# Performance work log

Measured on AMD Instinct MI355X. Metric: run time of the kernel, lower is better.

## Reference

```python
import jax, jax.numpy as jnp
import numpy as np

DIN, DK, DV, DR, NH, DMODEL = 512, 64, 64, 16, 8, 512
N = 4096
TOT = DK + DK + DV + DR  # per-head projection width = 208


def setup_inputs() -> dict:
    key = jax.random.key(0)
    k1, k2, k3, k4 = jax.random.split(key, 4)
    H = jax.random.normal(k1, (N, DIN), dtype=jnp.float32)
    D = jax.random.normal(k2, (N, N, DR), dtype=jnp.float32)
    attention_mask = jnp.zeros((N, N), dtype=jnp.float32)  # 0 = allowed
    # learned params (Linear, no bias): stored as [in, out] for x @ W
    W = jax.random.normal(k3, (DIN, NH * TOT), dtype=jnp.float32) / np.sqrt(DIN)
    Wout = jax.random.normal(k4, (NH * DV, DMODEL), dtype=jnp.float32) / np.sqrt(NH * DV)
    return {"H": H, "D": D, "attention_mask": attention_mask, "W": W, "Wout": Wout}


def reference(H, D, attention_mask, W, Wout):
    n = H.shape[0]
    # project and split into per-head Q, K, V, R: [h, n, *]
    H2 = (H @ W).reshape(n, NH, TOT).transpose(1, 0, 2)
    Q, K, V, R = jnp.split(H2, [DK, 2 * DK, 2 * DK + DV], axis=-1)
    # relative/route bias: RD[h,i,j] = sum_r R[h,i,r] * D[i,j,r]
    RD = jnp.einsum('hir,ijr->hij', R, D)
    scale = 1.0 / np.sqrt(DK + DR)
    scores = scale * (jnp.einsum('hid,hjd->hij', Q, K) + RD) + attention_mask
    probs = jax.nn.softmax(scores, axis=-1)
    ctx = jnp.einsum('hij,hjd->hid', probs, V)          # [h, n, dv]
    ctx = ctx.transpose(1, 0, 2).reshape(n, NH * DV)    # [n, h*dv]
    return ctx @ Wout                                    # [n, dmodel]
```

## Files before the change

kernel.cpp:

```cpp
#include <hip/hip_runtime.h>
#include <hip/hip_bf16.h>

#define NN 4096
#define NH 8
#define TOT 208
#define NPROJ 1664

typedef __attribute__((ext_vector_type(8))) short short8;
typedef __attribute__((ext_vector_type(4))) short short4_t;
typedef __attribute__((ext_vector_type(4))) float float4_t;

#define MFMA __builtin_amdgcn_mfma_f32_16x16x32_bf16

__device__ __forceinline__ short f2bf(float f){
  union { float f; unsigned u; } v; v.f = f;
  unsigned r = v.u + 0x7fffu + ((v.u >> 16) & 1u);
  return (short)(r >> 16);
}

__device__ __forceinline__ float bitsf(unsigned u){
  union { unsigned u; float f; } v; v.u = u; return v.f;
}

__device__ __forceinline__ short8 cvt8(float4_t a, float4_t b){
  union { short8 s; unsigned u[4]; } r;
  asm("v_cvt_pk_bf16_f32 %0, %1, %2" : "=v"(r.u[0]) : "v"(a[0]), "v"(a[1]));
  asm("v_cvt_pk_bf16_f32 %0, %1, %2" : "=v"(r.u[1]) : "v"(a[2]), "v"(a[3]));
  asm("v_cvt_pk_bf16_f32 %0, %1, %2" : "=v"(r.u[2]) : "v"(b[0]), "v"(b[1]));
  asm("v_cvt_pk_bf16_f32 %0, %1, %2" : "=v"(r.u[3]) : "v"(b[2]), "v"(b[3]));
  return r.s;
}

#define BAR() do{ \
    asm volatile("s_waitcnt lgkmcnt(0)" ::: "memory"); \
    __builtin_amdgcn_s_barrier(); \
    asm volatile("" ::: "memory"); \
  }while(0)

__global__ void k_cvt(const float* __restrict__ in, short* __restrict__ out, int n4){
  int i = blockIdx.x*256 + threadIdx.x;
  if(i >= n4) return;
  float4_t v = *(const float4_t*)(in + (size_t)i*4);
  short4_t o;
  o[0]=f2bf(v[0]); o[1]=f2bf(v[1]); o[2]=f2bf(v[2]); o[3]=f2bf(v[3]);
  *(short4_t*)(out + (size_t)i*4) = o;
}

__global__ void k_trans(const float* __restrict__ in, short* __restrict__ out, int R, int C){
  __shared__ float tile[32][33];
  int bc = blockIdx.x*32, br = blockIdx.y*32;
  int tx = threadIdx.x, ty = threadIdx.y;
  #pragma unroll
  for(int dy=0; dy<32; dy+=8){
    int r = br+ty+dy, c = bc+tx;
    if(r<R && c<C) tile[ty+dy][tx] = in[(size_t)r*C + c];
  }
  __syncthreads();
  #pragma unroll
  for(int dy=0; dy<32; dy+=8){
    int c = bc+ty+dy, r = br+tx;
    if(c<C && r<R) out[(size_t)c*R + r] = f2bf(tile[tx][ty+dy]);
  }
}

__global__ __launch_bounds__(256) void k_gemm(
    const short* __restrict__ A, const short* __restrict__ Bt, float* __restrict__ C,
    int M, int Ncols, int K)
{
  __shared__ __align__(16) short As[2][2048];
  __shared__ __align__(16) short Bs[2][2048];
  const int tid = threadIdx.x;
  const int l = tid & 63, w = tid >> 6;
  const int wm = w >> 1, wn = w & 1;
  const int g = l >> 4, i16 = l & 15;
  const size_t bm = (size_t)blockIdx.x * 64, bn = (size_t)blockIdx.y * 64;
  const int r = tid >> 2, cb = tid & 3;
  const int dst = r*32 + ((cb ^ (r&3))*8);
  const short* Ag = A + (bm + (size_t)r)*K + cb*8;
  const short* Bg = Bt + (bn + (size_t)r)*K + cb*8;
  float4_t z4 = {0.f,0.f,0.f,0.f};
  float4_t acc00=z4, acc01=z4, acc10=z4, acc11=z4;
  short8 ta = *(const short8*)(Ag);
  short8 tb = *(const short8*)(Bg);
  *(short8*)&As[0][dst] = ta;
  *(short8*)&Bs[0][dst] = tb;
  const int nk = K >> 5;
  int c = 0;
  const int swa = (g ^ (i16&3))*8;
  for(int kt=0; kt<nk; kt++){
    __syncthreads();
    if(kt+1 < nk){
      ta = *(const short8*)(Ag + (kt+1)*32);
      tb = *(const short8*)(Bg + (kt+1)*32);
    }
    short8 a0 = *(const short8*)&As[c][(wm*32 + i16)*32 + swa];
    short8 a1 = *(const short8*)&As[c][(wm*32 + 16 + i16)*32 + swa];
    short8 b0 = *(const short8*)&Bs[c][(wn*32 + i16)*32 + swa];
    short8 b1 = *(const short8*)&Bs[c][(wn*32 + 16 + i16)*32 + swa];
    acc00 = MFMA(a0,b0,acc00,0,0,0); acc01 = MFMA(a0,b1,acc01,0,0,0);
    acc10 = MFMA(a1,b0,acc10,0,0,0); acc11 = MFMA(a1,b1,acc11,0,0,0);
    if(kt+1 < nk){
      *(short8*)&As[c^1][dst] = ta;
      *(short8*)&Bs[c^1][dst] = tb;
    }
    c ^= 1;
  }
  #pragma unroll
  for(int rr=0; rr<4; rr++){
    C[(bm + wm*32 +      4*g + rr)*(size_t)Ncols + bn + wn*32 + i16]      = acc00[rr];
    C[(bm + wm*32 +      4*g + rr)*(size_t)Ncols + bn + wn*32 + 16 + i16] = acc01[rr];
    C[(bm + wm*32 + 16 + 4*g + rr)*(size_t)Ncols + bn + wn*32 + i16]      = acc10[rr];
    C[(bm + wm*32 + 16 + 4*g + rr)*(size_t)Ncols + bn + wn*32 + 16 + i16] = acc11[rr];
  }
}

__global__ void k_pack(const float* __restrict__ H2, short* __restrict__ Qp,
                       short* __restrict__ Kp, short* __restrict__ Vp, short* __restrict__ Rp){
  int T = blockIdx.x*256 + threadIdx.x;
  if(T < 262144){
    int l = T & 63; int rest = T >> 6;
    int kb = rest & 1; rest >>= 1;
    int it = rest & 255; int h = rest >> 8;
    int i = it*16 + (l & 15);
    int col = h*TOT + kb*32 + 8*(l>>4);
    const float* s = H2 + (size_t)i*NPROJ + col;
    short8 v;
    #pragma unroll
    for(int e=0;e<8;e++) v[e] = f2bf(s[e]);
    *(short8*)(Qp + (size_t)T*8) = v;
  } else if(T < 524288){
    int T2 = T - 262144;
    int l = T2 & 63; int rest = T2 >> 6;
    int kb = rest & 1; rest >>= 1;
    int it = rest & 255; int h = rest >> 8;
    int i = it*16 + (l & 15);
    int col = h*TOT + 64 + kb*32 + 8*(l>>4);
    const float* s = H2 + (size_t)i*NPROJ + col;
    short8 v;
    #pragma unroll
    for(int e=0;e<8;e++) v[e] = f2bf(s[e]);
    *(short8*)(Kp + (size_t)T2*8) = v;
  } else if(T < 786432){
    int T2 = T - 524288;
    int l = T2 & 63; int rest = T2 >> 6;
    int db = rest & 3; rest >>= 2;
    int jt = rest & 127; int h = rest >> 7;
    int col = h*TOT + 128 + db*16 + (l & 15);
    int j0 = jt*32 + 8*(l>>4);
    short8 v;
    #pragma unroll
    for(int e=0;e<8;e++) v[e] = f2bf(H2[(size_t)(j0+e)*NPROJ + col]);
    *(short8*)(Vp + (size_t)T2*8) = v;
  } else {
    int T2 = T - 786432;
    int half = T2 & 1; int hh = (T2>>1) & 15; int i = T2 >> 5;
    short8 v;
    #pragma unroll
    for(int e=0;e<8;e++) v[e] = 0;
    if(hh < 8){
      const float* s = H2 + (size_t)i*NPROJ + hh*TOT + 192 + half*8;
      #pragma unroll
      for(int e=0;e<8;e++) v[e] = f2bf(s[e]);
    }
    *(short8*)(Rp + (size_t)T2*8) = v;
  }
}

#define RDS2(h,j,i) (((h)*32+(j))*36+(i))
#define PS(ww,row,j) (((ww)*32+(row))*40+(j))

__global__ __launch_bounds__(512) void k_attn(
    const float* __restrict__ Dm, const float* __restrict__ mask,
    const short* __restrict__ Qp, const short* __restrict__ Kp,
    const short* __restrict__ Vp, const short* __restrict__ Rp,
    float* __restrict__ Opart, float* __restrict__ lpart)
{
  __shared__ __align__(16) short rdl[18432];
  __shared__ __align__(16) short p_lds[10240];

  const int tid = threadIdx.x;
  const int l = tid & 63, w = tid >> 6;
  const int g = l >> 4, i16 = l & 15;
  const int IT = blockIdx.x >> 1, jh = blockIdx.x & 1;
  const int i0 = IT * 32;
  const float iscale = 0.11180339887498949f;
  const float msc    = 8.944271909999159f;

  short8 qa[4];
  #pragma unroll
  for(int rg=0; rg<2; rg++)
    #pragma unroll
    for(int kb=0; kb<2; kb++)
      qa[rg*2+kb] = *(const short8*)(Qp + (((size_t)w*256 + IT*2+rg)*2 + kb)*512 + (size_t)l*8);

  short8 ra[4];
  #pragma unroll
  for(int row=0; row<4; row++)
    #pragma unroll
    for(int e=0; e<8; e++) ra[row][e] = 0;
  if(g < 2){
    #pragma unroll
    for(int row=0; row<4; row++)
      ra[row] = *(const short8*)(Rp + (size_t)(i0+4*w+row)*256 + i16*16 + 8*g);
  }

  float4_t z4 = {0.f,0.f,0.f,0.f};
  float4_t O[4][2];
  #pragma unroll
  for(int db=0; db<4; db++){ O[db][0]=z4; O[db][1]=z4; }
  float l_r[8];
  #pragma unroll
  for(int k2=0;k2<8;k2++) l_r[k2]=0.f;

  float4_t d[4][4];
  #pragma unroll
  for(int row=0; row<4; row++)
    #pragma unroll
    for(int q=0; q<4; q++) d[row][q] = z4;
  float mi[4][2];
  short8 kf[4], vf[4];

#define LOAD_D(tt) do{ if(g < 2){ \
    const float* dp0 = Dm + ((size_t)(i0+4*w+0)*NN + (size_t)(tt)*32 + i16)*16 + 8*g; \
    const float* dp1 = Dm + ((size_t)(i0+4*w+1)*NN + (size_t)(tt)*32 + i16)*16 + 8*g; \
    const float* dp2 = Dm + ((size_t)(i0+4*w+2)*NN + (size_t)(tt)*32 + i16)*16 + 8*g; \
    const float* dp3 = Dm + ((size_t)(i0+4*w+3)*NN + (size_t)(tt)*32 + i16)*16 + 8*g; \
    d[0][0]=*(const float4_t*)(dp0); d[0][1]=*(const float4_t*)(dp0+4); \
    d[0][2]=*(const float4_t*)(dp0+256); d[0][3]=*(const float4_t*)(dp0+260); \
    d[1][0]=*(const float4_t*)(dp1); d[1][1]=*(const float4_t*)(dp1+4); \
    d[1][2]=*(const float4_t*)(dp1+256); d[1][3]=*(const float4_t*)(dp1+260); \
    d[2][0]=*(const float4_t*)(dp2); d[2][1]=*(const float4_t*)(dp2+4); \
    d[2][2]=*(const float4_t*)(dp2+256); d[2][3]=*(const float4_t*)(dp2+260); \
    d[3][0]=*(const float4_t*)(dp3); d[3][1]=*(const float4_t*)(dp3+4); \
    d[3][2]=*(const float4_t*)(dp3+256); d[3][3]=*(const float4_t*)(dp3+260); \
  } }while(0)

#define LOAD_MI(tt) do{ \
    size_t jj = (size_t)(tt)*32 + i16; \
    mi[0][0] = mask[(size_t)(i0+4*w+0)*NN + jj] * msc; \
    mi[0][1] = mask[(size_t)(i0+4*w+0)*NN + jj + 16] * msc; \
    mi[1][0] = mask[(size_t)(i0+4*w+1)*NN + jj] * msc; \
    mi[1][1] = mask[(size_t)(i0+4*w+1)*NN + jj + 16] * msc; \
    mi[2][0] = mask[(size_t)(i0+4*w+2)*NN + jj] * msc; \
    mi[2][1] = mask[(size_t)(i0+4*w+2)*NN + jj + 16] * msc; \
    mi[3][0] = mask[(size_t)(i0+4*w+3)*NN + jj] * msc; \
    mi[3][1] = mask[(size_t)(i0+4*w+3)*NN + jj + 16] * msc; }while(0)

#define LOAD_K(tt) do{ \
    const short* kp = Kp + (((size_t)w*256 + (size_t)(tt)*2)*2)*512 + (size_t)l*8; \
    kf[0] = *(const short8*)(kp);        kf[1] = *(const short8*)(kp+512); \
    kf[2] = *(const short8*)(kp+1024);   kf[3] = *(const short8*)(kp+1536); }while(0)

#define LOAD_V(tt) do{ \
    const short* vp = Vp + (((size_t)w*128 + (size_t)(tt))*4)*512 + (size_t)l*8; \
    vf[0] = *(const short8*)(vp);        vf[1] = *(const short8*)(vp+512); \
    vf[2] = *(const short8*)(vp+1024);   vf[3] = *(const short8*)(vp+1536); }while(0)

  const int t0 = jh*64;
  LOAD_D(t0); LOAD_MI(t0); LOAD_K(t0); LOAD_V(t0);

  for(int t=0; t<64; t++){
    const int tt = t0 + t;
    const int tn = (t<63) ? tt+1 : tt;
    const int buf = (t&1)*8;
    #pragma unroll
    for(int row=0; row<4; row++){
      short8 df0 = cvt8(d[row][0], d[row][1]);
      short8 df1 = cvt8(d[row][2], d[row][3]);
      float4_t c0 = {mi[row][0],mi[row][0],mi[row][0],mi[row][0]};
      float4_t c1 = {mi[row][1],mi[row][1],mi[row][1],mi[row][1]};
      c0 = MFMA(ra[row], df0, c0,0,0,0);
      c1 = MFMA(ra[row], df1, c1,0,0,0);
      if(g < 2){
        int ib = 4*w + row;
        #pragma unroll
        for(int r=0; r<4; r++){
          rdl[RDS2(buf + 4*g+r, i16,    ib)] = f2bf(c0[r]);
          rdl[RDS2(buf + 4*g+r, 16+i16, ib)] = f2bf(c1[r]);
        }
      }
    }
    BAR();
    float4_t s[2][2];
    s[0][0] = MFMA(qa[0], kf[0], z4,0,0,0); s[0][0] = MFMA(qa[1], kf[1], s[0][0],0,0,0);
    s[0][1] = MFMA(qa[0], kf[2], z4,0,0,0); s[0][1] = MFMA(qa[1], kf[3], s[0][1],0,0,0);
    s[1][0] = MFMA(qa[2], kf[0], z4,0,0,0); s[1][0] = MFMA(qa[3], kf[1], s[1][0],0,0,0);
    s[1][1] = MFMA(qa[2], kf[2], z4,0,0,0); s[1][1] = MFMA(qa[3], kf[3], s[1][1],0,0,0);
    LOAD_D(tn); LOAD_MI(tn); LOAD_K(tn);
    float p[2][2][4];
    #pragma unroll
    for(int rg=0; rg<2; rg++){
      #pragma unroll
      for(int jg=0; jg<2; jg++){
        unsigned long long rv = *(const unsigned long long*)&rdl[RDS2(buf + w, jg*16+i16, rg*16+4*g)];
        unsigned lo = (unsigned)rv, hi = (unsigned)(rv>>32);
        float rf0 = bitsf(lo<<16), rf1 = bitsf(lo & 0xffff0000u);
        float rf2 = bitsf(hi<<16), rf3 = bitsf(hi & 0xffff0000u);
        p[rg][jg][0] = __expf((s[rg][jg][0] + rf0)*iscale);
        p[rg][jg][1] = __expf((s[rg][jg][1] + rf1)*iscale);
        p[rg][jg][2] = __expf((s[rg][jg][2] + rf2)*iscale);
        p[rg][jg][3] = __expf((s[rg][jg][3] + rf3)*iscale);
      }
      #pragma unroll
      for(int r=0; r<4; r++) l_r[rg*4+r] += p[rg][0][r] + p[rg][1][r];
    }
    #pragma unroll
    for(int rg=0; rg<2; rg++)
      #pragma unroll
      for(int jg=0; jg<2; jg++)
        #pragma unroll
        for(int r=0; r<4; r++)
          p_lds[PS(w, rg*16 + 4*g + r, jg*16 + i16)] = f2bf(p[rg][jg][r]);
    #pragma unroll
    for(int rg=0; rg<2; rg++){
      short8 pb = *(const short8*)&p_lds[PS(w, rg*16 + i16, 8*g)];
      O[0][rg] = MFMA(vf[0], pb, O[0][rg],0,0,0);
      O[1][rg] = MFMA(vf[1], pb, O[1][rg],0,0,0);
      O[2][rg] = MFMA(vf[2], pb, O[2][rg],0,0,0);
      O[3][rg] = MFMA(vf[3], pb, O[3][rg],0,0,0);
    }
    LOAD_V(tn);
  }
  #pragma unroll
  for(int dd=1; dd<16; dd<<=1)
    #pragma unroll
    for(int k2=0; k2<8; k2++) l_r[k2] += __shfl_xor(l_r[k2], dd);
  if(i16 == 0){
    #pragma unroll
    for(int rg=0; rg<2; rg++)
      #pragma unroll
      for(int r=0; r<4; r++)
        lpart[((size_t)jh*8 + w)*NN + i0 + rg*16 + 4*g + r] = l_r[rg*4+r];
  }
  #pragma unroll
  for(int rg=0; rg<2; rg++)
    #pragma unroll
    for(int db=0; db<4; db++)
      *(float4_t*)(Opart + ((size_t)jh*NN + i0 + rg*16 + i16)*512 + w*64 + db*16 + 4*g) = O[db][rg];
}

__global__ void k_merge(const float* __restrict__ Op, const float* __restrict__ lp,
                        short* __restrict__ ctx){
  int T = blockIdx.x*256 + threadIdx.x;
  int i = T >> 6; int c = (T & 63) * 8;
  int h = c >> 6;
  float lA = lp[(size_t)h*NN + i], lB = lp[(size_t)(8+h)*NN + i];
  float inv = 1.0f / (lA + lB);
  const float4_t* a = (const float4_t*)(Op + (size_t)i*512 + c);
  const float4_t* b = (const float4_t*)(Op + ((size_t)NN + i)*512 + c);
  float4_t x0 = a[0], x1 = a[1], y0 = b[0], y1 = b[1];
  short8 o;
  #pragma unroll
  for(int e=0; e<4; e++){
    o[e]   = f2bf((x0[e]+y0[e])*inv);
    o[e+4] = f2bf((x1[e]+y1[e])*inv);
  }
  *(short8*)(ctx + (size_t)i*512 + c) = o;
}

extern "C" void kernel_launch(void* const* d_in, const int* in_sizes, int n_in,
                              void* d_out, int out_size, void* d_ws, size_t ws_size,
                              hipStream_t stream) {
  (void)in_sizes; (void)n_in; (void)out_size; (void)ws_size;
  const float* H    = (const float*)d_in[0];
  const float* Dm   = (const float*)d_in[1];
  const float* mask = (const float*)d_in[2];
  const float* W    = (const float*)d_in[3];
  const float* Wout = (const float*)d_in[4];
  float* out = (float*)d_out;

  char* ws = (char*)d_ws;
  size_t off = 0;
  auto carve = [&](size_t bytes)->char*{
    char* p = ws + off; off += (bytes + 255) & ~(size_t)255; return p;
  };
  short* Hb    = (short*)carve((size_t)4096*512*2);
  short* Wt    = (short*)carve((size_t)1664*512*2);
  short* Wot   = (short*)carve((size_t)512*512*2);
  float* H2    = (float*)carve((size_t)4096*1664*4);
  short* Qp    = (short*)carve((size_t)8*256*2*64*8*2);
  short* Kp    = (short*)carve((size_t)8*256*2*64*8*2);
  short* Vp    = (short*)carve((size_t)8*128*4*64*8*2);
  short* Rp    = (short*)carve((size_t)4096*256*2);
  short* ctxb  = (short*)carve((size_t)4096*512*2);
  float* Opart = (float*)carve((size_t)2*4096*512*4);
  float* lp    = (float*)carve((size_t)2*8*4096*4);

  k_cvt<<<2048, 256, 0, stream>>>(H, Hb, 4096*512/4);
  k_trans<<<dim3(52,16), dim3(32,8), 0, stream>>>(W, Wt, 512, 1664);
  k_trans<<<dim3(16,16), dim3(32,8), 0, stream>>>(Wout, Wot, 512, 512);
  k_gemm<<<dim3(64,26), 256, 0, stream>>>(Hb, Wt, H2, 4096, 1664, 512);
  k_pack<<<3584, 256, 0, stream>>>(H2, Qp, Kp, Vp, Rp);
  k_attn<<<256, 512, 0, stream>>>(Dm, mask, Qp, Kp, Vp, Rp, Opart, lp);
  k_merge<<<1024, 256, 0, stream>>>(Opart, lp, ctxb);
  k_gemm<<<dim3(64,8), 256, 0, stream>>>(ctxb, Wot, out, 4096, 512, 512);
}
```

Baseline: 339.7 us.

## Stage D tiles through double-buffered LDS with all lanes loading coalesced

D loads now use all 64 lanes with contiguous float4 reads instead of only half the lanes doing strided loads. Each tile is converted to bf16 and written into a double-buffered LDS tile, and the MFMA operands are read back from LDS. Loads are issued two tiles ahead to hide more HBM latency. This adds 64KB of LDS and extra LDS traffic, which may lower occupancy.

```diff
diff --git a/kernel.cpp b/kernel.cpp
--- a/kernel.cpp
+++ b/kernel.cpp
@@ -20,15 +20,6 @@
 
 __device__ __forceinline__ float bitsf(unsigned u){
   union { unsigned u; float f; } v; v.u = u; return v.f;
-}
-
-__device__ __forceinline__ short8 cvt8(float4_t a, float4_t b){
-  union { short8 s; unsigned u[4]; } r;
-  asm("v_cvt_pk_bf16_f32 %0, %1, %2" : "=v"(r.u[0]) : "v"(a[0]), "v"(a[1]));
-  asm("v_cvt_pk_bf16_f32 %0, %1, %2" : "=v"(r.u[1]) : "v"(a[2]), "v"(a[3]));
-  asm("v_cvt_pk_bf16_f32 %0, %1, %2" : "=v"(r.u[2]) : "v"(b[0]), "v"(b[1]));
-  asm("v_cvt_pk_bf16_f32 %0, %1, %2" : "=v"(r.u[3]) : "v"(b[2]), "v"(b[3]));
-  return r.s;
 }
 
 #define BAR() do{ \
@@ -175,6 +166,7 @@
     const short* __restrict__ Vp, const short* __restrict__ Rp,
     float* __restrict__ Opart, float* __restrict__ lpart)
 {
+  __shared__ __align__(16) short Dlds[2*32*512];
   __shared__ __align__(16) short rdl[18432];
   __shared__ __align__(16) short p_lds[10240];
 
@@ -212,28 +204,33 @@
   #pragma unroll
   for(int k2=0;k2<8;k2++) l_r[k2]=0.f;
 
-  float4_t d[4][4];
-  #pragma unroll
-  for(int row=0; row<4; row++)
-    #pragma unroll
-    for(int q=0; q<4; q++) d[row][q] = z4;
+  float4_t gl[4][2];
   float mi[4][2];
   short8 kf[4], vf[4];
 
-#define LOAD_D(tt) do{ if(g < 2){ \
-    const float* dp0 = Dm + ((size_t)(i0+4*w+0)*NN + (size_t)(tt)*32 + i16)*16 + 8*g; \
-    const float* dp1 = Dm + ((size_t)(i0+4*w+1)*NN + (size_t)(tt)*32 + i16)*16 + 8*g; \
-    const float* dp2 = Dm + ((size_t)(i0+4*w+2)*NN + (size_t)(tt)*32 + i16)*16 + 8*g; \
-    const float* dp3 = Dm + ((size_t)(i0+4*w+3)*NN + (size_t)(tt)*32 + i16)*16 + 8*g; \
-    d[0][0]=*(const float4_t*)(dp0); d[0][1]=*(const float4_t*)(dp0+4); \
-    d[0][2]=*(const float4_t*)(dp0+256); d[0][3]=*(const float4_t*)(dp0+260); \
-    d[1][0]=*(const float4_t*)(dp1); d[1][1]=*(const float4_t*)(dp1+4); \
-    d[1][2]=*(const float4_t*)(dp1+256); d[1][3]=*(const float4_t*)(dp1+260); \
-    d[2][0]=*(const float4_t*)(dp2); d[2][1]=*(const float4_t*)(dp2+4); \
-    d[2][2]=*(const float4_t*)(dp2+256); d[2][3]=*(const float4_t*)(dp2+260); \
-    d[3][0]=*(const float4_t*)(dp3); d[3][1]=*(const float4_t*)(dp3+4); \
-    d[3][2]=*(const float4_t*)(dp3+256); d[3][3]=*(const float4_t*)(dp3+260); \
-  } }while(0)
+#define LOAD_GL(ts) do{ \
+    _Pragma("unroll") \
+    for(int row=0; row<4; row++){ \
+      const float* rb = Dm + ((size_t)(i0+4*w+row)*NN + (size_t)(ts)*32)*16; \
+      gl[row][0] = *(const float4_t*)(rb + l*4); \
+      gl[row][1] = *(const float4_t*)(rb + 256 + l*4); \
+    } }while(0)
+
+#define CVT_STORE(bufb) do{ \
+    short* dbp = Dlds + (bufb)*16384; \
+    const int jw = (l>>2), r0 = 4*(l&3); \
+    _Pragma("unroll") \
+    for(int row=0; row<4; row++){ \
+      _Pragma("unroll") \
+      for(int half=0; half<2; half++){ \
+        unsigned u0,u1; float4_t v = gl[row][half]; \
+        asm("v_cvt_pk_bf16_f32 %0, %1, %2" : "=v"(u0) : "v"(v[0]), "v"(v[1])); \
+        asm("v_cvt_pk_bf16_f32 %0, %1, %2" : "=v"(u1) : "v"(v[2]), "v"(v[3])); \
+        unsigned long long pk = (unsigned long long)u0 | ((unsigned long long)u1<<32); \
+        *(unsigned long long*)(dbp + (4*w+row)*512 + (half*16+jw)*16 + r0) = pk; \
+      } } \
+    asm volatile("" ::: "memory"); \
+  }while(0)
 
 #define LOAD_MI(tt) do{ \
     size_t jj = (size_t)(tt)*32 + i16; \
@@ -257,42 +254,54 @@
     vf[2] = *(const short8*)(vp+1024);   vf[3] = *(const short8*)(vp+1536); }while(0)
 
   const int t0 = jh*64;
-  LOAD_D(t0); LOAD_MI(t0); LOAD_K(t0); LOAD_V(t0);
+  LOAD_GL(t0);
+  LOAD_MI(t0); LOAD_K(t0); LOAD_V(t0);
+  CVT_STORE(0);
+  LOAD_GL(t0+1);
 
   for(int t=0; t<64; t++){
-    const int tt = t0 + t;
-    const int tn = (t<63) ? tt+1 : tt;
-    const int buf = (t&1)*8;
+    const int cur = t & 1;
+    const int tn = (t<63) ? t0+t+1 : t0+63;
+    const int tp = (t<62) ? t0+t+2 : t0+63;
+    const short* dcur = Dlds + cur*16384;
+    short8 zf;
+    #pragma unroll
+    for(int e=0;e<8;e++) zf[e] = 0;
     #pragma unroll
     for(int row=0; row<4; row++){
-      short8 df0 = cvt8(d[row][0], d[row][1]);
-      short8 df1 = cvt8(d[row][2], d[row][3]);
+      short8 db0 = zf, db1 = zf;
+      if(g < 2){
+        db0 = *(const short8*)(dcur + (4*w+row)*512 + i16*16      + 8*g);
+        db1 = *(const short8*)(dcur + (4*w+row)*512 + (16+i16)*16 + 8*g);
+      }
       float4_t c0 = {mi[row][0],mi[row][0],mi[row][0],mi[row][0]};
       float4_t c1 = {mi[row][1],mi[row][1],mi[row][1],mi[row][1]};
-      c0 = MFMA(ra[row], df0, c0,0,0,0);
-      c1 = MFMA(ra[row], df1, c1,0,0,0);
+      c0 = MFMA(ra[row], db0, c0,0,0,0);
+      c1 = MFMA(ra[row], db1, c1,0,0,0);
       if(g < 2){
         int ib = 4*w + row;
         #pragma unroll
         for(int r=0; r<4; r++){
-          rdl[RDS2(buf + 4*g+r, i16,    ib)] = f2bf(c0[r]);
-          rdl[RDS2(buf + 4*g+r, 16+i16, ib)] = f2bf(c1[r]);
+          rdl[RDS2(cur*8 + 4*g+r, i16,    ib)] = f2bf(c0[r]);
+          rdl[RDS2(cur*8 + 4*g+r, 16+i16, ib)] = f2bf(c1[r]);
         }
       }
     }
+    CVT_STORE(cur^1);
+    LOAD_GL(tp);
     BAR();
     float4_t s[2][2];
     s[0][0] = MFMA(qa[0], kf[0], z4,0,0,0); s[0][0] = MFMA(qa[1], kf[1], s[0][0],0,0,0);
     s[0][1] = MFMA(qa[0], kf[2], z4,0,0,0); s[0][1] = MFMA(qa[1], kf[3], s[0][1],0,0,0);
     s[1][0] = MFMA(qa[2], kf[0], z4,0,0,0); s[1][0] = MFMA(qa[3], kf[1], s[1][0],0,0,0);
     s[1][1] = MFMA(qa[2], kf[2], z4,0,0,0); s[1][1] = MFMA(qa[3], kf[3], s[1][1],0,0,0);
-    LOAD_D(tn); LOAD_MI(tn); LOAD_K(tn);
+    LOAD_MI(tn); LOAD_K(tn);
     float p[2][2][4];
     #pragma unroll
     for(int rg=0; rg<2; rg++){
       #pragma unroll
       for(int jg=0; jg<2; jg++){
-        unsigned long long rv = *(const unsigned long long*)&rdl[RDS2(buf + w, jg*16+i16, rg*16+4*g)];
+        unsigned long long rv = *(const unsigned long long*)&rdl[RDS2(cur*8 + w, jg*16+i16, rg*16+4*g)];
         unsigned lo = (unsigned)rv, hi = (unsigned)(rv>>32);
         float rf0 = bitsf(lo<<16), rf1 = bitsf(lo & 0xffff0000u);
         float rf2 = bitsf(hi<<16), rf3 = bitsf(hi & 0xffff0000u);
```

Result: faster. 288.3 us, median of 2 (-15.1%).
